# Optimization experiments

Measured on AMD Instinct MI355X. Metric: run time of the kernel, lower is better.

The kernel has to match this reference:

```python
import jax, jax.numpy as jnp
import numpy as np

# CUBA-LIF constants (from LavaNetwork.__init__ with beta=0.95)
THRESHOLD = 1.0
CURRENT_DECAY = 1.0   # current[t] = (1-1.0)*current[t-1] + input[t] == input[t]
VOLTAGE_DECAY = 1.0 - 0.95  # = 0.05, so v[t] = 0.95*v[t-1] + cur[t]

N_INPUT, N_HIDDEN, N_OUTPUT = 512, 2048, 4 * 64
B, T = 32, 1024


def setup_inputs() -> dict:
    key = jax.random.key(0)
    kx, k1, k2, k3, k4 = jax.random.split(key, 5)
    x = (jax.random.uniform(kx, (B, N_INPUT, T)) < 0.1).astype(jnp.float32)
    # learned params (Linear with bias); small scale so spiking is reasonable
    w1 = jax.random.normal(k1, (N_HIDDEN, N_INPUT), dtype=jnp.float32) * (1.0 / np.sqrt(N_INPUT))
    b1 = jax.random.normal(k2, (N_HIDDEN,), dtype=jnp.float32) * 0.01
    w2 = jax.random.normal(k3, (N_OUTPUT, N_HIDDEN), dtype=jnp.float32) * (1.0 / np.sqrt(N_HIDDEN))
    b2 = jax.random.normal(k4, (N_OUTPUT,), dtype=jnp.float32) * 0.01
    return {"x": x, "w1": w1, "b1": b1, "w2": w2, "b2": b2}


def _cuba_lif(cur):
    """CUBA neuron with current_decay=1 (current==synaptic input),
    leaky-integrate voltage, fire at threshold, reset voltage to 0.
    cur: (B, N, T) -> spikes (B, N, T)."""
    beta_v = 1.0 - VOLTAGE_DECAY  # 0.95

    def step(v, c_t):
        v = v * beta_v + c_t
        s = (v >= THRESHOLD).astype(v.dtype)
        v = v * (1.0 - s)  # reset-to-zero on spike (Loihi behavior)
        return v, s

    cur_t = jnp.moveaxis(cur, -1, 0)  # (T, B, N)
    v0 = jnp.zeros(cur.shape[:-1], cur.dtype)
    _, spk = jax.lax.scan(step, v0, cur_t)
    return jnp.moveaxis(spk, 0, -1)  # (B, N, T)


def reference(x, w1, b1, w2, b2):
    # layer 1: synapse (einsum 'bit,oi->bot' + bias) -> CUBA neuron
    cur1 = jnp.einsum('bit,oi->bot', x, w1) + b1[None, :, None]
    spk1 = _cuba_lif(cur1)
    # layer 2
    cur2 = jnp.einsum('bit,oi->bot', spk1, w2) + b2[None, :, None]
    spk2 = _cuba_lif(cur2)
    return (spk1, spk2)
```

## Files before the change

### kernel.cpp

```cpp
#include <hip/hip_runtime.h>


typedef int i32x4 __attribute__((ext_vector_type(4)));
typedef _Float16 f16x8 __attribute__((ext_vector_type(8)));
typedef _Float16 f16x4 __attribute__((ext_vector_type(4)));
typedef float f32x4 __attribute__((ext_vector_type(4)));

#define GLDS(g, l) __builtin_amdgcn_global_load_lds( \
    (const __attribute__((address_space(1))) void*)(g), \
    (__attribute__((address_space(3))) void*)(l), 16, 0, 0)

#define INV231 4.656612873077392578125e-10


__global__ __launch_bounds__(256) void prep_w8(const float* __restrict__ A,
                                               signed char* __restrict__ wp,
                                               int M, int K)
{
    long gt = (long)blockIdx.x * 256 + threadIdx.x;
    int kq4 = K >> 2;
    int m = (int)(gt / kq4), kq = (int)(gt % kq4);
    int k0 = kq * 4;
    int kt = k0 >> 6, kin = k0 & 63;
    int cw = ((kin >> 4) ^ (m >> 1)) & 3;
    float4 w = *(const float4*)&A[(long)m * K + k0];
    float wv[4] = {w.x, w.y, w.z, w.w};
    int pack[4] = {0, 0, 0, 0};
#pragma unroll
    for (int e = 0; e < 4; e++) {
        long k64 = (long)rint((double)wv[e] * 2147483648.0);
#pragma unroll
        for (int j = 0; j < 3; j++) {
            long r = ((k64 + 128) & 255) - 128;
            pack[j] |= ((int)r & 255) << (e * 8);
            k64 = (k64 - r) >> 8;
        }
        pack[3] |= ((int)k64 & 255) << (e * 8);
    }
#pragma unroll
    for (int p = 0; p < 4; p++)
        *(int*)&wp[(((long)kt * 4 + p) * M + m) * 64 + cw * 16 + (kin & 15)] = pack[p];
}

__global__ __launch_bounds__(256) void prep_x8(const float* __restrict__ x,
                                               unsigned char* __restrict__ xt)
{
    __shared__ float xs[64][68];
    const int b = blockIdx.z, i0 = blockIdx.y * 64, t0 = blockIdx.x * 64;
    const float* xb = x + ((long)b * 512 + i0) * 1024 + t0;
#pragma unroll
    for (int p = 0; p < 4; p++) {
        int f = threadIdx.x + p * 256;
        int i = f >> 4, t4 = (f & 15) * 4;
        *(float4*)&xs[i][t4] = *(const float4*)&xb[(long)i * 1024 + t4];
    }
    __syncthreads();
    int tt = threadIdx.x >> 2, c = threadIdx.x & 3;
    unsigned char bytes[16];
#pragma unroll
    for (int j = 0; j < 16; j++)
        bytes[j] = (unsigned char)xs[c * 16 + j][tt];
    *(uint4*)&xt[(((long)b * 8 + (i0 >> 6)) * 1024 + t0 + tt) * 64 + c * 16] =
        *(uint4*)bytes;
}

template <bool TRANS>
__global__ __launch_bounds__(256, 2) void gemm_i8(
    const signed char* __restrict__ wp,
    const unsigned char* __restrict__ act,
    const float* __restrict__ bias,
    float* __restrict__ C,
    int M, int K)
{
    __shared__ signed char Ws[2][4][32][64];

    const int b = blockIdx.y;
    const int m0 = blockIdx.z * 32, t0 = blockIdx.x * 256;
    const int tid = threadIdx.x, lane = tid & 63, wave = tid >> 6;
    const int wt = t0 + wave * 64;
    const int lm = lane & 15, lq = lane >> 4;
    const int fro = ((lq ^ (lm >> 1)) & 3) * 16;
    const int gl_t = lane >> 2, gl_c = (lane & 3) * 16;
    const int niter = K >> 6;

    const unsigned char* ab = act + (long)b * niter * 1024 * 64;
    const int p0 = wave >> 1, s0 = wave & 1;
    const int p1 = (wave + 4) >> 1, s1 = wave & 1;

    i32x4 acc[4][8];
#pragma unroll
    for (int p = 0; p < 4; p++)
#pragma unroll
        for (int q = 0; q < 8; q++) acc[p][q] = (i32x4)0;

    {
        const signed char* g0 = wp + (((long)p0) * M + m0 + s0 * 16 + gl_t) * 64 + gl_c;
        const signed char* g1 = wp + (((long)p1) * M + m0 + s1 * 16 + gl_t) * 64 + gl_c;
        GLDS(g0, &Ws[0][p0][s0 * 16][0]);
        GLDS(g1, &Ws[0][p1][s1 * 16][0]);
    }
    i32x4 a[4], an[4];
#pragma unroll
    for (int f = 0; f < 4; f++)
        a[f] = *(const i32x4*)&ab[((long)(wt + f * 16 + lm)) * 64 + lq * 16];
    __syncthreads();

    for (int it = 0; it < niter; it++) {
        const int buf = it & 1;
        const int nx = (it + 1 < niter) ? it + 1 : it;
        if (it + 1 < niter) {
            const long kb = (long)(it + 1) * 4;
            const signed char* g0 =
                wp + ((kb + p0) * M + m0 + s0 * 16 + gl_t) * 64 + gl_c;
            const signed char* g1 =
                wp + ((kb + p1) * M + m0 + s1 * 16 + gl_t) * 64 + gl_c;
            GLDS(g0, &Ws[buf ^ 1][p0][s0 * 16][0]);
            GLDS(g1, &Ws[buf ^ 1][p1][s1 * 16][0]);
        }
#pragma unroll
        for (int f = 0; f < 4; f++)
            an[f] = *(const i32x4*)&ab[((long)nx * 1024 + wt + f * 16 + lm) * 64 + lq * 16];

#pragma unroll
        for (int p = 0; p < 4; p++) {
            i32x4 w0 = *(const i32x4*)&Ws[buf][p][lm][fro];
            i32x4 w1 = *(const i32x4*)&Ws[buf][p][16 + lm][fro];
            if (TRANS) {
#pragma unroll
                for (int f = 0; f < 4; f++) {
                    acc[p][f * 2 + 0] = __builtin_amdgcn_mfma_i32_16x16x64_i8(
                        a[f], w0, acc[p][f * 2 + 0], 0, 0, 0);
                    acc[p][f * 2 + 1] = __builtin_amdgcn_mfma_i32_16x16x64_i8(
                        a[f], w1, acc[p][f * 2 + 1], 0, 0, 0);
                }
            } else {
#pragma unroll
                for (int f = 0; f < 4; f++) {
                    acc[p][0 + f] = __builtin_amdgcn_mfma_i32_16x16x64_i8(
                        w0, a[f], acc[p][0 + f], 0, 0, 0);
                    acc[p][4 + f] = __builtin_amdgcn_mfma_i32_16x16x64_i8(
                        w1, a[f], acc[p][4 + f], 0, 0, 0);
                }
            }
        }
        __syncthreads();
#pragma unroll
        for (int f = 0; f < 4; f++) a[f] = an[f];
    }

    if (TRANS) {
        double bv[2];
        bv[0] = (double)bias[m0 + lm];
        bv[1] = (double)bias[m0 + 16 + lm];
        float* Cb = C + (long)b * 1024 * M;
#pragma unroll
        for (int tf = 0; tf < 4; tf++)
#pragma unroll
            for (int r = 0; r < 4; r++) {
                const int trow = wt + tf * 16 + lq * 4 + r;
#pragma unroll
                for (int mf = 0; mf < 2; mf++) {
                    long T = acc[3][tf * 2 + mf][r];
                    T = T * 256 + acc[2][tf * 2 + mf][r];
                    T = T * 256 + acc[1][tf * 2 + mf][r];
                    T = T * 256 + acc[0][tf * 2 + mf][r];
                    Cb[(long)trow * M + m0 + mf * 16 + lm] =
                        (float)((double)T * INV231 + bv[mf]);
                }
            }
    } else {
        float* Cb = C + (long)b * M * 1024;
#pragma unroll
        for (int mf = 0; mf < 2; mf++)
#pragma unroll
            for (int r = 0; r < 4; r++) {
                const int mrow = m0 + mf * 16 + lq * 4 + r;
                const double bv = (double)bias[mrow];
#pragma unroll
                for (int tf = 0; tf < 4; tf++) {
                    long T = acc[3][mf * 4 + tf][r];
                    T = T * 256 + acc[2][mf * 4 + tf][r];
                    T = T * 256 + acc[1][mf * 4 + tf][r];
                    T = T * 256 + acc[0][mf * 4 + tf][r];
                    Cb[(long)mrow * 1024 + wt + tf * 16 + lm] =
                        (float)((double)T * INV231 + bv);
                }
            }
    }
}


__global__ __launch_bounds__(256) void lif1_t(
    const float* __restrict__ ct,
    unsigned char* __restrict__ spk8,
    unsigned* __restrict__ mask_ws)
{
    const int b = blockIdx.y;
    const int m = blockIdx.x * 256 + threadIdx.x;
    const float* src = ct + (long)b * 1024 * 2048 + m;
    unsigned char* spb = spk8 + (((long)b * 32 + (m >> 6)) * 1024) * 64 + (m & 63);
    unsigned* mw = mask_ws + (long)b * 32 * 2048 + m;
    double v = 0.0;
    float c0[32], c1[32];
#pragma unroll
    for (int j = 0; j < 32; j++)
        c0[j] = src[(long)j * 2048];
    for (int tw = 0; tw < 32; tw += 2) {
#pragma unroll
        for (int j = 0; j < 32; j++)
            c1[j] = src[(long)((tw + 1) * 32 + j) * 2048];
        unsigned mword = 0;
#pragma unroll
        for (int j = 0; j < 32; j++) {
            v = 0.95 * v + (double)c0[j];
            bool s = v >= 1.0;
            mword |= (s ? 1u : 0u) << j;
            if (s) v = 0.0;
            spb[(long)(tw * 32 + j) * 64] = s ? 1 : 0;
        }
        mw[(long)tw * 2048] = mword;
        if (tw + 2 < 32) {
#pragma unroll
            for (int j = 0; j < 32; j++)
                c0[j] = src[(long)((tw + 2) * 32 + j) * 2048];
        }
        mword = 0;
#pragma unroll
        for (int j = 0; j < 32; j++) {
            v = 0.95 * v + (double)c1[j];
            bool s = v >= 1.0;
            mword |= (s ? 1u : 0u) << j;
            if (s) v = 0.0;
            spb[(long)((tw + 1) * 32 + j) * 64] = s ? 1 : 0;
        }
        mw[(long)(tw + 1) * 2048] = mword;
    }
}

__global__ __launch_bounds__(256) void expand_spk(
    const unsigned* __restrict__ mask_ws,
    float* __restrict__ spk1)
{
    __shared__ unsigned msk[8][32];
    const long rowbase = (long)blockIdx.x * 8;
    const int b = (int)(rowbase >> 11), m0 = (int)(rowbase & 2047);
    const int tid = threadIdx.x;
    {
        int w = tid >> 3, r = tid & 7;
        msk[r][w] = mask_ws[((long)b * 32 + w) * 2048 + m0 + r];
    }
    __syncthreads();
    const int r = tid >> 5, l5 = tid & 31;
    float* dst = spk1 + (rowbase + r) * 1024;
    const int sh = (l5 & 7) * 4;
#pragma unroll
    for (int j = 0; j < 8; j++) {
        const int t = l5 * 4 + j * 128;
        const unsigned w = msk[r][(l5 >> 3) + j * 4];
        float4 o;
        o.x = ((w >> sh) & 1u) ? 1.f : 0.f;
        o.y = ((w >> (sh + 1)) & 1u) ? 1.f : 0.f;
        o.z = ((w >> (sh + 2)) & 1u) ? 1.f : 0.f;
        o.w = ((w >> (sh + 3)) & 1u) ? 1.f : 0.f;
        *(float4*)&dst[t] = o;
    }
}

template <int RPB>
__global__ __launch_bounds__(256) void lif_lds(float* __restrict__ cur)
{
    __shared__ float cs[RPB][36];
    const long rowbase = (long)blockIdx.x * RPB;
    float* base = cur + rowbase * 1024;
    const int tid = threadIdx.x;
    double v = 0.0;
    const int NV = RPB * 32 / 4;
    for (int tc = 0; tc < 1024; tc += 32) {
        for (int f = tid; f < NV; f += 256) {
            int row = f >> 3, t4 = (f & 7) * 4;
            *(float4*)&cs[row][t4] = *(const float4*)&base[(long)row * 1024 + tc + t4];
        }
        __syncthreads();
        if (tid < RPB) {
#pragma unroll
            for (int j = 0; j < 32; j++) {
                v = 0.95 * v + (double)cs[tid][j];
                bool s = v >= 1.0;
                cs[tid][j] = s ? 1.f : 0.f;
                if (s) v = 0.0;
            }
        }
        __syncthreads();
        for (int f = tid; f < NV; f += 256) {
            int row = f >> 3, t4 = (f & 7) * 4;
            *(float4*)&base[(long)row * 1024 + tc + t4] = *(float4*)&cs[row][t4];
        }
        __syncthreads();
    }
}


__device__ inline void split3(float w, _Float16& q0, _Float16& q1, _Float16& q2) {
    float p0 = rintf(w * 4096.f) * 2.44140625e-4f;
    float r1 = w - p0;
    float p1s = rintf(r1 * 8388608.f) * 2.44140625e-4f;
    float r2 = r1 - p1s * 4.8828125e-4f;
    float p2s = rintf(r2 * 1.7179869184e10f) * 1.220703125e-4f;
    q0 = (_Float16)p0; q1 = (_Float16)p1s; q2 = (_Float16)p2s;
}

__global__ __launch_bounds__(256) void gemm_f16x3_kernel(
    const float* __restrict__ A, const float* __restrict__ Bmat,
    const float* __restrict__ bias, float* __restrict__ C,
    int M, int N, int K, long sB, long sC)
{
    __shared__ _Float16 As[3][128][40];
    __shared__ _Float16 Bsh[128][40];
    const int batch = blockIdx.z;
    const float* Bp = Bmat + (long)batch * sB;
    float* Cp = C + (long)batch * sC;
    const int m0 = blockIdx.y * 128, n0 = blockIdx.x * 128;
    const int tid = threadIdx.x, lane = tid & 63, wave = tid >> 6;
    const int wrow = (wave >> 1) * 64, wcol = (wave & 1) * 64;
    const int lm = lane & 15, lq = lane >> 4;
    const int a_mo = tid >> 3, a_kc = (tid & 7) * 4;
    const int b_kq = tid >> 5, b_nq = tid & 31;

    f32x4 acc[3][4][4];
#pragma unroll
    for (int p = 0; p < 3; p++)
#pragma unroll
        for (int i = 0; i < 4; i++)
#pragma unroll
            for (int j = 0; j < 4; j++) acc[p][i][j] = (f32x4)0.f;

    for (int k0 = 0; k0 < K; k0 += 32) {
#pragma unroll
        for (int i = 0; i < 4; i++) {
            const int m = i * 32 + a_mo;
            float4 w = *(const float4*)&A[(long)(m0 + m) * K + k0 + a_kc];
            _Float16 a0[4], a1[4], a2[4];
            split3(w.x, a0[0], a1[0], a2[0]);
            split3(w.y, a0[1], a1[1], a2[1]);
            split3(w.z, a0[2], a1[2], a2[2]);
            split3(w.w, a0[3], a1[3], a2[3]);
            *(f16x4*)&As[0][m][a_kc] = (f16x4){a0[0], a0[1], a0[2], a0[3]};
            *(f16x4*)&As[1][m][a_kc] = (f16x4){a1[0], a1[1], a1[2], a1[3]};
            *(f16x4*)&As[2][m][a_kc] = (f16x4){a2[0], a2[1], a2[2], a2[3]};
        }
        {
            float4 r0 = *(const float4*)&Bp[(long)(k0 + b_kq * 4 + 0) * N + n0 + b_nq * 4];
            float4 r1 = *(const float4*)&Bp[(long)(k0 + b_kq * 4 + 1) * N + n0 + b_nq * 4];
            float4 r2 = *(const float4*)&Bp[(long)(k0 + b_kq * 4 + 2) * N + n0 + b_nq * 4];
            float4 r3 = *(const float4*)&Bp[(long)(k0 + b_kq * 4 + 3) * N + n0 + b_nq * 4];
            *(f16x4*)&Bsh[b_nq * 4 + 0][b_kq * 4] =
                (f16x4){(_Float16)r0.x, (_Float16)r1.x, (_Float16)r2.x, (_Float16)r3.x};
            *(f16x4*)&Bsh[b_nq * 4 + 1][b_kq * 4] =
                (f16x4){(_Float16)r0.y, (_Float16)r1.y, (_Float16)r2.y, (_Float16)r3.y};
            *(f16x4*)&Bsh[b_nq * 4 + 2][b_kq * 4] =
                (f16x4){(_Float16)r0.z, (_Float16)r1.z, (_Float16)r2.z, (_Float16)r3.z};
            *(f16x4*)&Bsh[b_nq * 4 + 3][b_kq * 4] =
                (f16x4){(_Float16)r0.w, (_Float16)r1.w, (_Float16)r2.w, (_Float16)r3.w};
        }
        __syncthreads();
        f16x8 bf[4];
#pragma unroll
        for (int j = 0; j < 4; j++)
            bf[j] = *(const f16x8*)&Bsh[wcol + j * 16 + lm][lq * 8];
#pragma unroll
        for (int p = 0; p < 3; p++) {
            f16x8 af[4];
#pragma unroll
            for (int i = 0; i < 4; i++)
                af[i] = *(const f16x8*)&As[p][wrow + i * 16 + lm][lq * 8];
#pragma unroll
            for (int i = 0; i < 4; i++)
#pragma unroll
                for (int j = 0; j < 4; j++)
                    acc[p][i][j] = __builtin_amdgcn_mfma_f32_16x16x32_f16(
                        af[i], bf[j], acc[p][i][j], 0, 0, 0);
        }
        __syncthreads();
    }
#pragma unroll
    for (int i = 0; i < 4; i++)
#pragma unroll
        for (int r = 0; r < 4; r++) {
            const int row = m0 + wrow + i * 16 + lq * 4 + r;
            const double bv = (double)bias[row];
#pragma unroll
            for (int j = 0; j < 4; j++) {
                double s = (double)acc[0][i][j][r]
                         + (double)acc[1][i][j][r] * 4.8828125e-4
                         + (double)acc[2][i][j][r] * 4.76837158203125e-7 + bv;
                Cp[(long)row * N + n0 + wcol + j * 16 + lm] = (float)s;
            }
        }
}

__global__ __launch_bounds__(256) void lif_rows(float* __restrict__ data,
                                                long nrows, int T)
{
    long r = (long)blockIdx.x * blockDim.x + threadIdx.x;
    if (r >= nrows) return;
    float* p = data + r * (long)T;
    double v = 0.0;
    for (int t = 0; t < T; t += 4) {
        float4 c = *(float4*)(p + t);
        float4 s;
        v = 0.95 * v + (double)c.x; s.x = (v >= 1.0) ? 1.f : 0.f; if (v >= 1.0) v = 0.0;
        v = 0.95 * v + (double)c.y; s.y = (v >= 1.0) ? 1.f : 0.f; if (v >= 1.0) v = 0.0;
        v = 0.95 * v + (double)c.z; s.z = (v >= 1.0) ? 1.f : 0.f; if (v >= 1.0) v = 0.0;
        v = 0.95 * v + (double)c.w; s.w = (v >= 1.0) ? 1.f : 0.f; if (v >= 1.0) v = 0.0;
        *(float4*)(p + t) = s;
    }
}


extern "C" void kernel_launch(void* const* d_in, const int* in_sizes, int n_in,
                              void* d_out, int out_size, void* d_ws, size_t ws_size,
                              hipStream_t stream)
{
    const float* x  = (const float*)d_in[0];
    const float* w1 = (const float*)d_in[1];
    const float* b1 = (const float*)d_in[2];
    const float* w2 = (const float*)d_in[3];
    const float* b2 = (const float*)d_in[4];

    float* out  = (float*)d_out;
    float* spk1 = out;
    float* spk2 = out + (long)32 * 2048 * 1024;

    const size_t WP1 = 4194304;
    const size_t WP2 = 2097152;
    const size_t X8T = 16777216;
    const size_t SPK = 67108864;
    const size_t MSK = 8388608;
    const size_t NEED = WP1 + WP2 + X8T + SPK + MSK;

    if (ws_size >= NEED) {
        char* ws = (char*)d_ws;
        signed char* wp1 = (signed char*)ws;
        signed char* wp2 = (signed char*)(ws + WP1);
        unsigned char* x8t = (unsigned char*)(ws + WP1 + WP2);
        unsigned char* spk8 = (unsigned char*)(ws + WP1 + WP2 + X8T);
        unsigned* mask_ws = (unsigned*)(ws + WP1 + WP2 + X8T + SPK);

        prep_w8<<<1024, 256, 0, stream>>>(w1, wp1, 2048, 512);
        prep_w8<<<512, 256, 0, stream>>>(w2, wp2, 256, 2048);
        prep_x8<<<dim3(16, 8, 32), 256, 0, stream>>>(x, x8t);

        gemm_i8<true><<<dim3(4, 32, 64), 256, 0, stream>>>(
            wp1, x8t, b1, spk1, 2048, 512);
        lif1_t<<<dim3(8, 32), 256, 0, stream>>>(spk1, spk8, mask_ws);
        expand_spk<<<8192, 256, 0, stream>>>(mask_ws, spk1);

        gemm_i8<false><<<dim3(4, 32, 8), 256, 0, stream>>>(
            wp2, spk8, b2, spk2, 256, 2048);
        lif_lds<32><<<256, 256, 0, stream>>>(spk2);
    } else {
        gemm_f16x3_kernel<<<dim3(8, 16, 32), 256, 0, stream>>>(
            w1, x, b1, spk1, 2048, 1024, 512, (long)512 * 1024, (long)2048 * 1024);
        lif_rows<<<(65536 + 255) / 256, 256, 0, stream>>>(spk1, 65536, 1024);
        gemm_f16x3_kernel<<<dim3(8, 2, 32), 256, 0, stream>>>(
            w2, spk1, b2, spk2, 256, 1024, 2048, (long)2048 * 1024, (long)256 * 1024);
        lif_rows<<<(8192 + 255) / 256, 256, 0, stream>>>(spk2, 8192, 1024);
    }
}
```

Baseline: 743.4 us.

## Stage weight K-chunks into LDS in bulk instead of per-iteration double buffering

The int8 GEMM now takes NITER and CHUNK as template parameters and loads CHUNK K-tiles of weights into LDS at once (all 8 for layer 1, 4 chunks of 8 for layer 2), replacing the per-iteration double-buffered LDS load with its barrier on every iteration. Activation registers are double-buffered explicitly and the k loop is fully unrolled. This removes most __syncthreads and address arithmetic, but weight loads are no longer overlapped with MFMA between chunks, and LDS use grows to 64KB per block, which can lower occupancy.

```diff
diff --git a/kernel.cpp b/kernel.cpp
--- a/kernel.cpp
+++ b/kernel.cpp
@@ -64,15 +64,16 @@
         *(uint4*)bytes;
 }
 
-template <bool TRANS>
+template <bool TRANS, int NITER, int CHUNK>
 __global__ __launch_bounds__(256, 2) void gemm_i8(
     const signed char* __restrict__ wp,
     const unsigned char* __restrict__ act,
     const float* __restrict__ bias,
     float* __restrict__ C,
-    int M, int K)
-{
-    __shared__ signed char Ws[2][4][32][64];
+    int M)
+{
+    constexpr int NCHUNK = NITER / CHUNK;
+    __shared__ signed char Ws[CHUNK][4][32][64];
 
     const int b = blockIdx.y;
     const int m0 = blockIdx.z * 32, t0 = blockIdx.x * 256;
@@ -80,12 +81,21 @@
     const int wt = t0 + wave * 64;
     const int lm = lane & 15, lq = lane >> 4;
     const int fro = ((lq ^ (lm >> 1)) & 3) * 16;
-    const int gl_t = lane >> 2, gl_c = (lane & 3) * 16;
-    const int niter = K >> 6;
-
-    const unsigned char* ab = act + (long)b * niter * 1024 * 64;
-    const int p0 = wave >> 1, s0 = wave & 1;
-    const int p1 = (wave + 4) >> 1, s1 = wave & 1;
+    const int gl_row = lane >> 2, gl_col = (lane & 3) * 16;
+
+    const unsigned char* ab = act + (long)b * NITER * 1024 * 64;
+
+    auto stage = [&](int cc) {
+#pragma unroll
+        for (int j = 0; j < CHUNK; ++j) {
+            const int r = wave + 4 * j;
+            const int kt = r >> 2, p = r & 3;
+            const long kg = ((long)(cc * CHUNK + kt) * 4 + p);
+            const signed char* g = wp + (kg * M + m0 + gl_row) * 64 + gl_col;
+            GLDS(g, &Ws[kt][p][0][0]);
+            GLDS(g + 16 * 64, &Ws[kt][p][16][0]);
+        }
+    };
 
     i32x4 acc[4][8];
 #pragma unroll
@@ -93,59 +103,52 @@
 #pragma unroll
         for (int q = 0; q < 8; q++) acc[p][q] = (i32x4)0;
 
-    {
-        const signed char* g0 = wp + (((long)p0) * M + m0 + s0 * 16 + gl_t) * 64 + gl_c;
-        const signed char* g1 = wp + (((long)p1) * M + m0 + s1 * 16 + gl_t) * 64 + gl_c;
-        GLDS(g0, &Ws[0][p0][s0 * 16][0]);
-        GLDS(g1, &Ws[0][p1][s1 * 16][0]);
-    }
-    i32x4 a[4], an[4];
+    stage(0);
+    i32x4 areg[2][4];
 #pragma unroll
     for (int f = 0; f < 4; f++)
-        a[f] = *(const i32x4*)&ab[((long)(wt + f * 16 + lm)) * 64 + lq * 16];
+        areg[0][f] = *(const i32x4*)&ab[((long)(wt + f * 16 + lm)) * 64 + lq * 16];
     __syncthreads();
 
-    for (int it = 0; it < niter; it++) {
-        const int buf = it & 1;
-        const int nx = (it + 1 < niter) ? it + 1 : it;
-        if (it + 1 < niter) {
-            const long kb = (long)(it + 1) * 4;
-            const signed char* g0 =
-                wp + ((kb + p0) * M + m0 + s0 * 16 + gl_t) * 64 + gl_c;
-            const signed char* g1 =
-                wp + ((kb + p1) * M + m0 + s1 * 16 + gl_t) * 64 + gl_c;
-            GLDS(g0, &Ws[buf ^ 1][p0][s0 * 16][0]);
-            GLDS(g1, &Ws[buf ^ 1][p1][s1 * 16][0]);
-        }
-#pragma unroll
-        for (int f = 0; f < 4; f++)
-            an[f] = *(const i32x4*)&ab[((long)nx * 1024 + wt + f * 16 + lm) * 64 + lq * 16];
-
-#pragma unroll
-        for (int p = 0; p < 4; p++) {
-            i32x4 w0 = *(const i32x4*)&Ws[buf][p][lm][fro];
-            i32x4 w1 = *(const i32x4*)&Ws[buf][p][16 + lm][fro];
-            if (TRANS) {
-#pragma unroll
-                for (int f = 0; f < 4; f++) {
-                    acc[p][f * 2 + 0] = __builtin_amdgcn_mfma_i32_16x16x64_i8(
-                        a[f], w0, acc[p][f * 2 + 0], 0, 0, 0);
-                    acc[p][f * 2 + 1] = __builtin_amdgcn_mfma_i32_16x16x64_i8(
-                        a[f], w1, acc[p][f * 2 + 1], 0, 0, 0);
+    for (int c = 0; c < NCHUNK; ++c) {
+#pragma unroll
+        for (int kk = 0; kk < CHUNK; ++kk) {
+            {
+                const int itv = c * CHUNK + kk;
+                const long nx = (itv + 1 < NITER) ? itv + 1 : itv;
+#pragma unroll
+                for (int f = 0; f < 4; f++)
+                    areg[(kk + 1) & 1][f] = *(const i32x4*)
+                        &ab[(nx * 1024 + wt + f * 16 + lm) * 64 + lq * 16];
+            }
+#pragma unroll
+            for (int p = 0; p < 4; p++) {
+                i32x4 w0 = *(const i32x4*)&Ws[kk][p][lm][fro];
+                i32x4 w1 = *(const i32x4*)&Ws[kk][p][16 + lm][fro];
+                if (TRANS) {
+#pragma unroll
+                    for (int f = 0; f < 4; f++) {
+                        acc[p][f * 2 + 0] = __builtin_amdgcn_mfma_i32_16x16x64_i8(
+                            areg[kk & 1][f], w0, acc[p][f * 2 + 0], 0, 0, 0);
+                        acc[p][f * 2 + 1] = __builtin_amdgcn_mfma_i32_16x16x64_i8(
+                            areg[kk & 1][f], w1, acc[p][f * 2 + 1], 0, 0, 0);
+                    }
+                } else {
+#pragma unroll
+                    for (int f = 0; f < 4; f++) {
+                        acc[p][0 + f] = __builtin_amdgcn_mfma_i32_16x16x64_i8(
+                            w0, areg[kk & 1][f], acc[p][0 + f], 0, 0, 0);
+                        acc[p][4 + f] = __builtin_amdgcn_mfma_i32_16x16x64_i8(
+                            w1, areg[kk & 1][f], acc[p][4 + f], 0, 0, 0);
+                    }
                 }
-            } else {
-#pragma unroll
-                for (int f = 0; f < 4; f++) {
-                    acc[p][0 + f] = __builtin_amdgcn_mfma_i32_16x16x64_i8(
-                        w0, a[f], acc[p][0 + f], 0, 0, 0);
-                    acc[p][4 + f] = __builtin_amdgcn_mfma_i32_16x16x64_i8(
-                        w1, a[f], acc[p][4 + f], 0, 0, 0);
-                }
-            }
-        }
-        __syncthreads();
-#pragma unroll
-        for (int f = 0; f < 4; f++) a[f] = an[f];
+            }
+        }
+        if (c + 1 < NCHUNK) {
+            __syncthreads();
+            stage(c + 1);
+            __syncthreads();
+        }
     }
 
     if (TRANS) {
@@ -450,13 +453,13 @@
         prep_w8<<<512, 256, 0, stream>>>(w2, wp2, 256, 2048);
         prep_x8<<<dim3(16, 8, 32), 256, 0, stream>>>(x, x8t);
 
-        gemm_i8<true><<<dim3(4, 32, 64), 256, 0, stream>>>(
-            wp1, x8t, b1, spk1, 2048, 512);
+        gemm_i8<true, 8, 8><<<dim3(4, 32, 64), 256, 0, stream>>>(
+            wp1, x8t, b1, spk1, 2048);
         lif1_t<<<dim3(8, 32), 256, 0, stream>>>(spk1, spk8, mask_ws);
         expand_spk<<<8192, 256, 0, stream>>>(mask_ws, spk1);
 
-        gemm_i8<false><<<dim3(4, 32, 8), 256, 0, stream>>>(
-            wp2, spk8, b2, spk2, 256, 2048);
+        gemm_i8<false, 32, 8><<<dim3(4, 32, 8), 256, 0, stream>>>(
+            wp2, spk8, b2, spk2, 256);
         lif_lds<32><<<256, 256, 0, stream>>>(spk2);
     } else {
         gemm_f16x3_kernel<<<dim3(8, 16, 32), 256, 0, stream>>>(
```

New measurement: 684.1 us. 8.0% less time.
